# Kernel optimization log

Hardware: AMD Instinct MI355X
Metric: run time of the kernel (lower is better)

The kernel has to match this reference:

```python
import jax, jax.numpy as jnp
import numpy as np

N = 524288          # batch of embedded samples
K = 16              # num_mixtures
D = 16              # dimension_embedding


def setup_inputs() -> dict:
    key = jax.random.key(0)
    k_s, k_phi, k_mu, k_sig = jax.random.split(key, 4)
    samples = jax.random.normal(k_s, (N, D), dtype=jnp.float32)
    # Mixture.__init__: Phi ~ U[0,1) scalar per mixture, mu ~ 2*U[0,1)-0.5
    Phi = jax.random.uniform(k_phi, (K,), dtype=jnp.float32)
    mu = 2.0 * jax.random.uniform(k_mu, (K, D), dtype=jnp.float32) - 0.5
    # Sigma init is identity in the original; use a well-conditioned SPD
    # perturbation of identity so inverse/det are non-trivial but stable.
    A = jax.random.normal(k_sig, (K, D, D), dtype=jnp.float32)
    Sigma = jnp.eye(D, dtype=jnp.float32)[None] + 0.1 * jnp.einsum('kij,klj->kil', A, A) / D
    return {"samples": samples, "Phi": Phi, "mu": mu, "Sigma": Sigma}


def reference(samples, Phi, mu, Sigma):
    # Faithful batched version of GMM.forward: sum_k Phi_k * exp(-0.5 * diff^T Sigma_k^{-1} diff) / sqrt(2*pi*det(Sigma_k)), then -log.
    inv_sigma = jnp.linalg.inv(Sigma)                      # [K, D, D]
    det_sigma = jnp.linalg.det(Sigma)                      # [K]
    diff = samples[None, :, :] - mu[:, None, :]            # [K, N, D]
    quad = jnp.einsum('knd,kde,kne->kn', diff, inv_sigma, diff)  # [K, N]
    # NOTE: original normalizes by sqrt(2*pi*det), not (2*pi)^{D/2}*sqrt(det);
    # we reproduce the original math exactly.
    norm = jnp.sqrt(2.0 * jnp.pi * det_sigma)[:, None]     # [K, 1]
    pdf = Phi[:, None] * jnp.exp(-0.5 * quad) / norm       # [K, N]
    return -jnp.log(jnp.sum(pdf, axis=0))                  # [N]
```

## Files before the change

kernel.cpp:

```cpp
#include <hip/hip_runtime.h>
#include <hip/hip_bf16.h>
#include <math.h>

#define KMIX 16
#define DIM  16
#define TPW  8
#define TRI_IDX(i,j) (((i)*((i)+1))/2 + (j))

typedef _Float16 half8 __attribute__((ext_vector_type(8)));
typedef float    f32x4 __attribute__((ext_vector_type(4)));

__global__ __launch_bounds__(64) void gmm_precompute(
    const float* __restrict__ Phi, const float* __restrict__ mu,
    const float* __restrict__ Sigma,
    _Float16* __restrict__ wsA, float* __restrict__ wsC)
{
    __shared__ float sLi[KMIX][DIM][DIM];
    __shared__ float sNB[KMIX][DIM];
    const int lane = threadIdx.x;

    if (lane < KMIX) {
        const int k = lane;
        float a[136], rd[DIM];

        #pragma unroll
        for (int i = 0; i < DIM; ++i)
            #pragma unroll
            for (int j = 0; j <= i; ++j)
                a[TRI_IDX(i, j)] = Sigma[k * 256 + i * 16 + j];

        #pragma unroll
        for (int i = 0; i < DIM; ++i) {
            #pragma unroll
            for (int j = 0; j <= i; ++j) {
                float s = a[TRI_IDX(i, j)];
                #pragma unroll
                for (int m = 0; m < j; ++m)
                    s -= a[TRI_IDX(i, m)] * a[TRI_IDX(j, m)];
                if (j == i) {
                    const float d = __builtin_amdgcn_sqrtf(s);
                    a[TRI_IDX(i, i)] = d;
                    rd[i] = __builtin_amdgcn_rcpf(d);
                } else {
                    a[TRI_IDX(i, j)] = s * rd[j];
                }
            }
        }

        #pragma unroll
        for (int c = 0; c < DIM; ++c) {
            a[TRI_IDX(c, c)] = rd[c];
            #pragma unroll
            for (int r = c + 1; r < DIM; ++r) {
                float s = 0.0f;
                #pragma unroll
                for (int m = c; m < r; ++m)
                    s += a[TRI_IDX(r, m)] * a[TRI_IDX(m, c)];
                a[TRI_IDX(r, c)] = -s * rd[r];
            }
        }

        float invd = 1.0f;
        #pragma unroll
        for (int i = 0; i < DIM; ++i) invd *= rd[i];
        wsC[k] = Phi[k] * 0.3989422804014327f * invd;

        float mv[DIM];
        #pragma unroll
        for (int j = 0; j < DIM; ++j) mv[j] = mu[k * DIM + j];
        #pragma unroll
        for (int r = 0; r < DIM; ++r) {
            float b = 0.0f;
            #pragma unroll
            for (int j = 0; j <= r; ++j) b += a[TRI_IDX(r, j)] * mv[j];
            sNB[k][r] = -b;
            #pragma unroll
            for (int j = 0; j < DIM; ++j)
                sLi[k][r][j] = (j <= r) ? a[TRI_IDX(r, j)] : 0.0f;
        }
    }
    __syncthreads();

    const int m = lane & 15;
    const int quad = lane >> 4;
    for (int mix = 0; mix < KMIX; ++mix) {
        half8 h;
        #pragma unroll
        for (int j = 0; j < 8; ++j) {
            float v;
            if (quad == 0)      v = sLi[mix][m][j];
            else if (quad == 1) v = sLi[mix][m][8 + j];
            else if (quad == 2) v = (j == 0) ? sNB[mix][m] : 0.0f;
            else                v = 0.0f;
            h[j] = (_Float16)v;
        }
        ((half8*)wsA)[mix * 64 + lane] = h;
    }
}

__global__ __launch_bounds__(256) void gmm_main(
    const float* __restrict__ samples,
    const _Float16* __restrict__ wsA, const float* __restrict__ wsC,
    float* __restrict__ out, int N, int ntiles)
{
    const int lane = threadIdx.x & 63;
    const int wave = blockIdx.x * (blockDim.x >> 6) + (threadIdx.x >> 6);
    const int n = lane & 15;
    const int quad = lane >> 4;

    half8 afrag[KMIX];
    #pragma unroll
    for (int mix = 0; mix < KMIX; ++mix)
        afrag[mix] = ((const half8*)wsA)[mix * 64 + lane];
    float ck[KMIX];
    #pragma unroll
    for (int mix = 0; mix < KMIX; ++mix) ck[mix] = wsC[mix];

    const f32x4 zero = {0.0f, 0.0f, 0.0f, 0.0f};

    for (int t = 0; t < TPW; ++t) {
        const int tile = wave * TPW + t;
        if (tile >= ntiles) break;
        const int s0 = tile * 16;

        half8 bfrag;
        #pragma unroll
        for (int j = 0; j < 8; ++j) bfrag[j] = (_Float16)0.0f;
        if (quad < 2) {
            int sidx = s0 + n; if (sidx >= N) sidx = N - 1;
            const float4* p = (const float4*)(samples + (size_t)sidx * DIM + quad * 8);
            const float4 u = p[0], v = p[1];
            bfrag[0] = (_Float16)u.x; bfrag[1] = (_Float16)u.y;
            bfrag[2] = (_Float16)u.z; bfrag[3] = (_Float16)u.w;
            bfrag[4] = (_Float16)v.x; bfrag[5] = (_Float16)v.y;
            bfrag[6] = (_Float16)v.z; bfrag[7] = (_Float16)v.w;
        } else if (quad == 2) {
            bfrag[0] = (_Float16)1.0f;
        }

        float sum = 0.0f;
        #pragma unroll
        for (int mix = 0; mix < KMIX; ++mix) {
            const f32x4 d = __builtin_amdgcn_mfma_f32_16x16x32_f16(
                afrag[mix], bfrag, zero, 0, 0, 0);
            float q = d[0] * d[0];
            q = fmaf(d[1], d[1], q);
            q = fmaf(d[2], d[2], q);
            q = fmaf(d[3], d[3], q);
            q += __shfl_xor(q, 16, 64);
            q += __shfl_xor(q, 32, 64);
            sum = fmaf(ck[mix], __expf(-0.5f * q), sum);
        }

        const int sidx = s0 + n;
        if (quad == 0 && sidx < N) out[sidx] = -__logf(sum);
    }
}

extern "C" void kernel_launch(void* const* d_in, const int* in_sizes, int n_in,
                              void* d_out, int out_size, void* d_ws, size_t ws_size,
                              hipStream_t stream)
{
    const float* samples = (const float*)d_in[0];
    const float* Phi     = (const float*)d_in[1];
    const float* mu      = (const float*)d_in[2];
    const float* Sigma   = (const float*)d_in[3];
    float* out = (float*)d_out;
    const int N = in_sizes[0] / DIM;

    _Float16* wsA = (_Float16*)d_ws;
    float* wsC = (float*)((char*)d_ws + KMIX * 64 * 8 * sizeof(_Float16));

    gmm_precompute<<<1, 64, 0, stream>>>(Phi, mu, Sigma, wsA, wsC);

    const int ntiles = (N + 15) / 16;
    const int waves  = (ntiles + TPW - 1) / TPW;
    const int blocks = (waves + 3) / 4;
    gmm_main<<<blocks, 256, 0, stream>>>(samples, wsA, wsC, out, N, ntiles);
}
```

Baseline: 107.1 us.

## Fuse per-mixture Cholesky precompute into main GMM kernel per block

Removes the separate single-block precompute launch and its workspace round trip by having every block of the main kernel compute the inverse Cholesky factors, normalizers and offsets into shared memory, then build MFMA fragments locally. This removes a kernel launch and serial dependency between kernels. In exchange every block redundantly repeats the serial triangular factorization on 16 threads, adds shared memory use, and raises register pressure under a 256-thread launch bound.

New measurement: 197.6 us. 1.85x slower.

```diff
diff --git a/kernel.cpp b/kernel.cpp
--- a/kernel.cpp
+++ b/kernel.cpp
@@ -10,17 +10,20 @@
 typedef _Float16 half8 __attribute__((ext_vector_type(8)));
 typedef float    f32x4 __attribute__((ext_vector_type(4)));
 
-__global__ __launch_bounds__(64) void gmm_precompute(
+__global__ __launch_bounds__(256) void gmm_fused(
+    const float* __restrict__ samples,
     const float* __restrict__ Phi, const float* __restrict__ mu,
     const float* __restrict__ Sigma,
-    _Float16* __restrict__ wsA, float* __restrict__ wsC)
+    float* __restrict__ out, int N, int ntiles)
 {
     __shared__ float sLi[KMIX][DIM][DIM];
     __shared__ float sNB[KMIX][DIM];
-    const int lane = threadIdx.x;
+    __shared__ float sCk[KMIX];
 
-    if (lane < KMIX) {
-        const int k = lane;
+    const int tid = threadIdx.x;
+
+    if (tid < KMIX) {
+        const int k = tid;
         float a[136], rd[DIM];
 
         #pragma unroll
@@ -63,7 +66,7 @@
         float invd = 1.0f;
         #pragma unroll
         for (int i = 0; i < DIM; ++i) invd *= rd[i];
-        wsC[k] = Phi[k] * 0.3989422804014327f * invd;
+        sCk[k] = Phi[k] * 0.3989422804014327f * invd;
 
         float mv[DIM];
         #pragma unroll
@@ -81,8 +84,14 @@
     }
     __syncthreads();
 
-    const int m = lane & 15;
+    const int lane = tid & 63;
+    const int wave = blockIdx.x * 4 + (tid >> 6);
+    const int n = lane & 15;
     const int quad = lane >> 4;
+    const int m = n;
+
+    half8 afrag[KMIX];
+    #pragma unroll
     for (int mix = 0; mix < KMIX; ++mix) {
         half8 h;
         #pragma unroll
@@ -94,27 +103,11 @@
             else                v = 0.0f;
             h[j] = (_Float16)v;
         }
-        ((half8*)wsA)[mix * 64 + lane] = h;
+        afrag[mix] = h;
     }
-}
-
-__global__ __launch_bounds__(256) void gmm_main(
-    const float* __restrict__ samples,
-    const _Float16* __restrict__ wsA, const float* __restrict__ wsC,
-    float* __restrict__ out, int N, int ntiles)
-{
-    const int lane = threadIdx.x & 63;
-    const int wave = blockIdx.x * (blockDim.x >> 6) + (threadIdx.x >> 6);
-    const int n = lane & 15;
-    const int quad = lane >> 4;
-
-    half8 afrag[KMIX];
-    #pragma unroll
-    for (int mix = 0; mix < KMIX; ++mix)
-        afrag[mix] = ((const half8*)wsA)[mix * 64 + lane];
     float ck[KMIX];
     #pragma unroll
-    for (int mix = 0; mix < KMIX; ++mix) ck[mix] = wsC[mix];
+    for (int mix = 0; mix < KMIX; ++mix) ck[mix] = sCk[mix];
 
     const f32x4 zero = {0.0f, 0.0f, 0.0f, 0.0f};
 
@@ -168,13 +161,9 @@
     float* out = (float*)d_out;
     const int N = in_sizes[0] / DIM;
 
-    _Float16* wsA = (_Float16*)d_ws;
-    float* wsC = (float*)((char*)d_ws + KMIX * 64 * 8 * sizeof(_Float16));
-
-    gmm_precompute<<<1, 64, 0, stream>>>(Phi, mu, Sigma, wsA, wsC);
-
     const int ntiles = (N + 15) / 16;
     const int waves  = (ntiles + TPW - 1) / TPW;
     const int blocks = (waves + 3) / 4;
-    gmm_main<<<blocks, 256, 0, stream>>>(samples, wsA, wsC, out, N, ntiles);
+
+    gmm_fused<<<blocks, 256, 0, stream>>>(samples, Phi, mu, Sigma, out, N, ntiles);
 }
```

## Parallelize Cholesky and triangular inverse across lanes in precompute kernel

Applied to the files above, without the earlier changes.

The per-mixture Cholesky factorization and lower-triangular inversion, previously done serially by one thread per mixture with a 136-entry register array, are now spread so that each lane owns one row. Lanes exchange pivots and columns through wave shuffles, and the work runs across 4 blocks of 4 mixtures each. The shared-memory staging pass and its barrier are removed, and the MFMA A-fragments are written directly. This targets the serial latency of the single-thread precompute launch, at the cost of many cross-lane shuffles.

After: 99.86 us (median of 2 runs). 1.07x faster.

```diff
diff --git a/kernel.cpp b/kernel.cpp
--- a/kernel.cpp
+++ b/kernel.cpp
@@ -5,7 +5,6 @@
 #define KMIX 16
 #define DIM  16
 #define TPW  8
-#define TRI_IDX(i,j) (((i)*((i)+1))/2 + (j))
 
 typedef _Float16 half8 __attribute__((ext_vector_type(8)));
 typedef float    f32x4 __attribute__((ext_vector_type(4)));
@@ -15,87 +14,85 @@
     const float* __restrict__ Sigma,
     _Float16* __restrict__ wsA, float* __restrict__ wsC)
 {
-    __shared__ float sLi[KMIX][DIM][DIM];
-    __shared__ float sNB[KMIX][DIM];
     const int lane = threadIdx.x;
+    const int r    = lane & 15;
+    const int base = lane & 48;
+    const int k    = blockIdx.x * 4 + (lane >> 4);
 
-    if (lane < KMIX) {
-        const int k = lane;
-        float a[136], rd[DIM];
+    float l[DIM];
+    {
+        const float4* p = (const float4*)(Sigma + k * 256 + r * 16);
+        const float4 a = p[0], b = p[1], c = p[2], d = p[3];
+        l[0]=a.x;  l[1]=a.y;  l[2]=a.z;  l[3]=a.w;
+        l[4]=b.x;  l[5]=b.y;  l[6]=b.z;  l[7]=b.w;
+        l[8]=c.x;  l[9]=c.y;  l[10]=c.z; l[11]=c.w;
+        l[12]=d.x; l[13]=d.y; l[14]=d.z; l[15]=d.w;
+    }
 
+    float rd_own = 0.0f;
+    #pragma unroll
+    for (int j = 0; j < DIM; ++j) {
+        const float dj  = __builtin_amdgcn_sqrtf(l[j]);
+        const float rdj = __builtin_amdgcn_rcpf(dj);
+        if (r == j) { l[j] = dj; rd_own = rdj; }
+        const float rdb = __shfl(rdj, base + j, 64);
+        if (r > j) l[j] *= rdb;
         #pragma unroll
-        for (int i = 0; i < DIM; ++i)
-            #pragma unroll
-            for (int j = 0; j <= i; ++j)
-                a[TRI_IDX(i, j)] = Sigma[k * 256 + i * 16 + j];
-
-        #pragma unroll
-        for (int i = 0; i < DIM; ++i) {
-            #pragma unroll
-            for (int j = 0; j <= i; ++j) {
-                float s = a[TRI_IDX(i, j)];
-                #pragma unroll
-                for (int m = 0; m < j; ++m)
-                    s -= a[TRI_IDX(i, m)] * a[TRI_IDX(j, m)];
-                if (j == i) {
-                    const float d = __builtin_amdgcn_sqrtf(s);
-                    a[TRI_IDX(i, i)] = d;
-                    rd[i] = __builtin_amdgcn_rcpf(d);
-                } else {
-                    a[TRI_IDX(i, j)] = s * rd[j];
-                }
-            }
-        }
-
-        #pragma unroll
-        for (int c = 0; c < DIM; ++c) {
-            a[TRI_IDX(c, c)] = rd[c];
-            #pragma unroll
-            for (int r = c + 1; r < DIM; ++r) {
-                float s = 0.0f;
-                #pragma unroll
-                for (int m = c; m < r; ++m)
-                    s += a[TRI_IDX(r, m)] * a[TRI_IDX(m, c)];
-                a[TRI_IDX(r, c)] = -s * rd[r];
-            }
-        }
-
-        float invd = 1.0f;
-        #pragma unroll
-        for (int i = 0; i < DIM; ++i) invd *= rd[i];
-        wsC[k] = Phi[k] * 0.3989422804014327f * invd;
-
-        float mv[DIM];
-        #pragma unroll
-        for (int j = 0; j < DIM; ++j) mv[j] = mu[k * DIM + j];
-        #pragma unroll
-        for (int r = 0; r < DIM; ++r) {
-            float b = 0.0f;
-            #pragma unroll
-            for (int j = 0; j <= r; ++j) b += a[TRI_IDX(r, j)] * mv[j];
-            sNB[k][r] = -b;
-            #pragma unroll
-            for (int j = 0; j < DIM; ++j)
-                sLi[k][r][j] = (j <= r) ? a[TRI_IDX(r, j)] : 0.0f;
+        for (int c = j + 1; c < DIM; ++c) {
+            const float Lcj = __shfl(l[j], base + c, 64);
+            if (r >= c) l[c] = fmaf(-l[j], Lcj, l[c]);
         }
     }
-    __syncthreads();
 
-    const int m = lane & 15;
-    const int quad = lane >> 4;
-    for (int mix = 0; mix < KMIX; ++mix) {
-        half8 h;
+    float v[DIM], acc[DIM];
+    #pragma unroll
+    for (int c = 0; c < DIM; ++c) { v[c] = 0.0f; acc[c] = 0.0f; }
+    #pragma unroll
+    for (int m = 0; m < DIM; ++m) {
+        if (r == m) {
+            #pragma unroll
+            for (int c = 0; c < DIM; ++c)
+                if (c < m) v[c] = -rd_own * acc[c];
+            v[m] = rd_own;
+        }
         #pragma unroll
-        for (int j = 0; j < 8; ++j) {
-            float v;
-            if (quad == 0)      v = sLi[mix][m][j];
-            else if (quad == 1) v = sLi[mix][m][8 + j];
-            else if (quad == 2) v = (j == 0) ? sNB[mix][m] : 0.0f;
-            else                v = 0.0f;
-            h[j] = (_Float16)v;
+        for (int c = 0; c <= m; ++c) {
+            const float Vmc = __shfl(v[c], base + m, 64);
+            if (r > m) acc[c] = fmaf(l[m], Vmc, acc[c]);
         }
-        ((half8*)wsA)[mix * 64 + lane] = h;
     }
+
+    float prod = rd_own;
+    prod *= __shfl_xor(prod, 1, 64);
+    prod *= __shfl_xor(prod, 2, 64);
+    prod *= __shfl_xor(prod, 4, 64);
+    prod *= __shfl_xor(prod, 8, 64);
+    if (r == 0) wsC[k] = Phi[k] * 0.3989422804014327f * prod;
+
+    float b = 0.0f;
+    {
+        const float4* pm = (const float4*)(mu + k * DIM);
+        const float4 m0 = pm[0], m1 = pm[1], m2 = pm[2], m3 = pm[3];
+        const float mv[DIM] = {m0.x,m0.y,m0.z,m0.w, m1.x,m1.y,m1.z,m1.w,
+                               m2.x,m2.y,m2.z,m2.w, m3.x,m3.y,m3.z,m3.w};
+        #pragma unroll
+        for (int c = 0; c < DIM; ++c) b = fmaf(v[c], mv[c], b);
+    }
+
+    half8 h0, h1, h2, h3;
+    #pragma unroll
+    for (int j = 0; j < 8; ++j) {
+        h0[j] = (_Float16)v[j];
+        h1[j] = (_Float16)v[8 + j];
+        h2[j] = (_Float16)0.0f;
+        h3[j] = (_Float16)0.0f;
+    }
+    h2[0] = (_Float16)(-b);
+    half8* W = (half8*)wsA + k * 64;
+    W[r]      = h0;
+    W[16 + r] = h1;
+    W[32 + r] = h2;
+    W[48 + r] = h3;
 }
 
 __global__ __launch_bounds__(256) void gmm_main(
@@ -171,7 +168,7 @@
     _Float16* wsA = (_Float16*)d_ws;
     float* wsC = (float*)((char*)d_ws + KMIX * 64 * 8 * sizeof(_Float16));
 
-    gmm_precompute<<<1, 64, 0, stream>>>(Phi, mu, Sigma, wsA, wsC);
+    gmm_precompute<<<4, 64, 0, stream>>>(Phi, mu, Sigma, wsA, wsC);
 
     const int ntiles = (N + 15) / 16;
     const int waves  = (ntiles + TPW - 1) / TPW;
```
